# Performance work log

Measured on AMD Instinct MI355X. Metric: run time of the kernel, lower is better.

The kernel has to match this reference:

```python
import jax, jax.numpy as jnp
import numpy as np

N_NODES = 100000
N_EDGES = 3200000
F_IN = 256
HID = 64
N_CLS = 16


def setup_inputs() -> dict:
    key = jax.random.key(0)
    ks = jax.random.split(key, 12)
    x = jax.random.normal(ks[0], (N_NODES, F_IN), dtype=jnp.float32)
    edge_index = jax.random.randint(ks[1], (2, N_EDGES), 0, N_NODES, dtype=jnp.int32)
    w_mul = jax.random.normal(ks[2], (N_EDGES, 1), dtype=jnp.float32)
    s1 = 1.0 / np.sqrt(F_IN)
    s2 = 1.0 / np.sqrt(HID)
    # layer 1 params
    lin1_w = jax.random.uniform(ks[3], (HID, F_IN), minval=-s1, maxval=s1, dtype=jnp.float32)
    lin1_b = jax.random.uniform(ks[4], (HID,), minval=-s1, maxval=s1, dtype=jnp.float32)
    mlp1_w0 = jax.random.uniform(ks[5], (HID, 1), minval=-1.0, maxval=1.0, dtype=jnp.float32)
    mlp1_w1 = jax.random.uniform(ks[6], (HID, HID), minval=-s2, maxval=s2, dtype=jnp.float32)
    mlp1_b1 = jax.random.uniform(ks[7], (HID,), minval=-s2, maxval=s2, dtype=jnp.float32)
    # layer 2 params
    lin2_w = jax.random.uniform(ks[8], (N_CLS, HID), minval=-s2, maxval=s2, dtype=jnp.float32)
    lin2_b = jax.random.uniform(ks[9], (N_CLS,), minval=-s2, maxval=s2, dtype=jnp.float32)
    mlp2_w0 = jax.random.uniform(ks[10], (HID, 1), minval=-1.0, maxval=1.0, dtype=jnp.float32)
    mlp2_w1 = jax.random.uniform(ks[11], (N_CLS, HID), minval=-s2, maxval=s2, dtype=jnp.float32)
    mlp2_b1 = jnp.zeros((N_CLS,), dtype=jnp.float32)
    return dict(x=x, edge_index=edge_index, w_mul=w_mul,
                lin1_w=lin1_w, lin1_b=lin1_b, mlp1_w0=mlp1_w0, mlp1_w1=mlp1_w1, mlp1_b1=mlp1_b1,
                lin2_w=lin2_w, lin2_b=lin2_b, mlp2_w0=mlp2_w0, mlp2_w1=mlp2_w1, mlp2_b1=mlp2_b1)


def curv_layer(x, src, dst, w_mul, lin_w, lin_b, m_w0, m_w1, m_b1, n_nodes):
    # dense projection: [N, out]
    h = x @ lin_w.T + lin_b
    # per-edge weight MLP: Linear(1,HID,no bias) -> LeakyReLU(0.2) -> Linear(HID,out,bias)
    ew = jax.nn.leaky_relu(w_mul @ m_w0.T, negative_slope=0.2) @ m_w1.T + m_b1  # [E, out]
    # segment softmax keyed by source node (PyG softmax(out_weight, edge_index[0]))
    emax = jax.ops.segment_max(ew, src, num_segments=n_nodes)  # [N, out]
    e = jnp.exp(ew - emax[src])
    esum = jax.ops.segment_sum(e, src, num_segments=n_nodes)
    alpha = e / (esum[src] + 1e-16)  # [E, out]
    # message = alpha * x_j (x_j = h[src]); scatter-add at destination
    msg = alpha * h[src]
    return jax.ops.segment_sum(msg, dst, num_segments=n_nodes)  # [N, out]


def reference(x, edge_index, w_mul,
              lin1_w, lin1_b, mlp1_w0, mlp1_w1, mlp1_b1,
              lin2_w, lin2_b, mlp2_w0, mlp2_w1, mlp2_b1):
    src, dst = edge_index[0], edge_index[1]
    n = x.shape[0]
    # eval mode: dropout(p=0.8) is identity
    h = curv_layer(x, src, dst, w_mul, lin1_w, lin1_b, mlp1_w0, mlp1_w1, mlp1_b1, n)
    h = jax.nn.elu(h)
    h = curv_layer(h, src, dst, w_mul, lin2_w, lin2_b, mlp2_w0, mlp2_w1, mlp2_b1, n)
    return jax.nn.log_softmax(h, axis=1)
```

## Files before the change

### kernel.cpp

```cpp
#include <hip/hip_runtime.h>
#include <math.h>

#define FIN 256
#define HID 64
#define NCLS 16
#define BSH 8
#define BWD (1 << BSH)
#define NBKMAX 512
#define CAP 9216
#define CHUNK_S 16384
#define CHUNK_D 8192

typedef __attribute__((ext_vector_type(8))) short bf16x8;
typedef __attribute__((ext_vector_type(4))) float f32x4;

__global__ __launch_bounds__(512) void init_kernel(int* gcur_s, int* gcur_d) {
    int tid = threadIdx.x;
    gcur_s[tid] = tid * CAP;
    gcur_d[tid] = tid * CAP;
}

__global__ __launch_bounds__(512) void stage_kernel(const int* __restrict__ ei,
                                                    const float* __restrict__ w,
                                                    int* gcur_s, int* gcur_d,
                                                    unsigned int* st_s, uint2* st_d,
                                                    int E, int nchunk_s) {
    __shared__ int lh[NBKMAX];
    __shared__ int lofs[NBKMAX];
    __shared__ int lcur[NBKMAX];
    __shared__ int gbase[NBKMAX];
    __shared__ uint2 buf2[CHUNK_D];
    unsigned int* buf1 = (unsigned int*)buf2;
    int tid = threadIdx.x;
    int side = (blockIdx.x >= nchunk_s) ? 1 : 0;
    lh[tid] = 0;
    __syncthreads();
    if (!side) {
        int base = blockIdx.x * CHUNK_S;
        #pragma unroll
        for (int j = 0; j < CHUNK_S / 512; j++) {
            int e = base + tid + j * 512;
            if (e < E) atomicAdd(&lh[((unsigned)ei[e]) >> BSH], 1);
        }
    } else {
        int base = (blockIdx.x - nchunk_s) * CHUNK_D;
        #pragma unroll
        for (int j = 0; j < CHUNK_D / 512; j++) {
            int e = base + tid + j * 512;
            if (e < E) atomicAdd(&lh[((unsigned)ei[E + e]) >> BSH], 1);
        }
    }
    __syncthreads();
    int v = lh[tid];
    lofs[tid] = v;
    __syncthreads();
    for (int off = 1; off < 512; off <<= 1) {
        int add = (tid >= off) ? lofs[tid - off] : 0;
        __syncthreads();
        lofs[tid] += add;
        __syncthreads();
    }
    int ex = lofs[tid] - v;
    lofs[tid] = ex;
    lcur[tid] = ex;
    __syncthreads();
    if (!side) {
        int base = blockIdx.x * CHUNK_S;
        #pragma unroll
        for (int j = 0; j < CHUNK_S / 512; j++) {
            int e = base + tid + j * 512;
            if (e < E) {
                int s = ei[e];
                unsigned int rec = (__float_as_uint(w[e]) & 0xFFFFFF00u) | (unsigned int)(s & 0xFF);
                int p = atomicAdd(&lcur[((unsigned)s) >> BSH], 1);
                buf1[p] = rec;
            }
        }
    } else {
        int base = (blockIdx.x - nchunk_s) * CHUNK_D;
        #pragma unroll
        for (int j = 0; j < CHUNK_D / 512; j++) {
            int e = base + tid + j * 512;
            if (e < E) {
                int d = ei[E + e];
                int s = ei[e];
                unsigned int rec = (__float_as_uint(w[e]) & 0xFFFFFF00u) | (unsigned int)(d & 0xFF);
                int p = atomicAdd(&lcur[((unsigned)d) >> BSH], 1);
                buf2[p] = make_uint2((unsigned int)s, rec);
            }
        }
    }
    __syncthreads();
    {
        int c = lh[tid];
        if (c) gbase[tid] = atomicAdd(side ? &gcur_d[tid] : &gcur_s[tid], c);
    }
    __syncthreads();
    int wv = tid >> 6, lane = tid & 63;
    if (!side) {
        for (int b = wv; b < NBKMAX; b += 8) {
            int c = lh[b];
            int ls = lofs[b], gs = gbase[b];
            for (int i = lane; i < c; i += 64) st_s[gs + i] = buf1[ls + i];
        }
    } else {
        for (int b = wv; b < NBKMAX; b += 8) {
            int c = lh[b];
            int ls = lofs[b], gs = gbase[b];
            for (int i = lane; i < c; i += 64) st_d[gs + i] = buf2[ls + i];
        }
    }
}

__global__ __launch_bounds__(512) void bucket_scan_kernel(const int* gcur_s, const int* gcur_d,
                                                          int* bbase_s, int* bbase_d,
                                                          int* offs_s, int* offs_d,
                                                          int N, int nbk, int E) {
    int side = blockIdx.x;
    const int* gc = side ? gcur_d : gcur_s;
    int* bb = side ? bbase_d : bbase_s;
    __shared__ int tmp[512];
    int tid = threadIdx.x;
    int v = (tid < nbk) ? (gc[tid] - tid * CAP) : 0;
    tmp[tid] = v;
    __syncthreads();
    for (int off = 1; off < 512; off <<= 1) {
        int add = (tid >= off) ? tmp[tid - off] : 0;
        __syncthreads();
        tmp[tid] += add;
        __syncthreads();
    }
    if (tid < nbk) bb[tid] = tmp[tid] - v;
    if (tid == 0) {
        bb[nbk] = E;
        (side ? offs_d : offs_s)[N] = E;
    }
}

__global__ __launch_bounds__(256) void bucket_build_s_kernel(const int* __restrict__ bbase,
                                                             const unsigned int* __restrict__ st,
                                                             int* offs, float* t_s, int N) {
    int b = blockIdx.x;
    int r0 = bbase[b];
    int cnt = bbase[b + 1] - r0;
    if (cnt > CAP) cnt = CAP;
    size_t sb = (size_t)b * CAP;
    int n0 = b << BSH;
    int nn = min(BWD, N - n0);
    __shared__ int lh[BWD];
    __shared__ int lofs[BWD];
    __shared__ float buf[CAP];
    int tid = threadIdx.x;
    lh[tid] = 0;
    __syncthreads();
    for (int i = tid; i < cnt; i += 256) atomicAdd(&lh[st[sb + i] & 0xFFu], 1);
    __syncthreads();
    int v = lh[tid];
    lofs[tid] = v;
    __syncthreads();
    for (int off = 1; off < 256; off <<= 1) {
        int add = (tid >= off) ? lofs[tid - off] : 0;
        __syncthreads();
        lofs[tid] += add;
        __syncthreads();
    }
    int ex = lofs[tid] - v;
    if (tid < nn) offs[n0 + tid] = r0 + ex;
    lofs[tid] = ex;
    __syncthreads();
    for (int i = tid; i < cnt; i += 256) {
        unsigned int rec = st[sb + i];
        int p = atomicAdd(&lofs[rec & 0xFFu], 1);
        buf[p] = __uint_as_float(rec & 0xFFFFFF00u);
    }
    __syncthreads();
    for (int i = tid; i < cnt; i += 256) t_s[r0 + i] = buf[i];
}

__global__ __launch_bounds__(256) void bucket_build_d_kernel(const int* __restrict__ bbase,
                                                             const uint2* __restrict__ st,
                                                             int* offs, int2* ed, int N) {
    int b = blockIdx.x;
    int r0 = bbase[b];
    int cnt = bbase[b + 1] - r0;
    if (cnt > CAP) cnt = CAP;
    size_t sb = (size_t)b * CAP;
    int n0 = b << BSH;
    int nn = min(BWD, N - n0);
    __shared__ int lh[BWD];
    __shared__ int lofs[BWD];
    __shared__ int2 buf[CAP];
    int tid = threadIdx.x;
    lh[tid] = 0;
    __syncthreads();
    for (int i = tid; i < cnt; i += 256) atomicAdd(&lh[st[sb + i].y & 0xFFu], 1);
    __syncthreads();
    int v = lh[tid];
    lofs[tid] = v;
    __syncthreads();
    for (int off = 1; off < 256; off <<= 1) {
        int add = (tid >= off) ? lofs[tid - off] : 0;
        __syncthreads();
        lofs[tid] += add;
        __syncthreads();
    }
    int ex = lofs[tid] - v;
    if (tid < nn) offs[n0 + tid] = r0 + ex;
    lofs[tid] = ex;
    __syncthreads();
    for (int i = tid; i < cnt; i += 256) {
        uint2 rec = st[sb + i];
        int p = atomicAdd(&lofs[rec.y & 0xFFu], 1);
        buf[p] = make_int2((int)rec.x, (int)(rec.y & 0xFFFFFF00u));
    }
    __syncthreads();
    for (int i = tid; i < cnt; i += 256) ed[r0 + i] = buf[i];
}

#define LOG2E 1.44269504088896340736f
__global__ void prep_kernel(const float* __restrict__ w0a, const float* __restrict__ w1a,
                            const float* __restrict__ w0b, const float* __restrict__ w1b,
                            float* Ap1, float* An1, float* Ap2, float* An2) {
    int tid = threadIdx.x;
    if (tid < 64) {
        float ap = 0.f, an = 0.f;
        for (int j = 0; j < 64; j++) {
            float w0 = w0a[j];
            float w1 = w1a[tid * 64 + j];
            ap += w0 * ((w0 >= 0.f) ? 1.f : 0.2f) * w1;
            an += w0 * ((w0 <= 0.f) ? 1.f : 0.2f) * w1;
        }
        Ap1[tid] = ap * LOG2E; An1[tid] = an * LOG2E;
    } else if (tid < 80) {
        int k = tid - 64;
        float ap = 0.f, an = 0.f;
        for (int j = 0; j < 64; j++) {
            float w0 = w0b[j];
            float w1 = w1b[k * 64 + j];
            ap += w0 * ((w0 >= 0.f) ? 1.f : 0.2f) * w1;
            an += w0 * ((w0 <= 0.f) ? 1.f : 0.2f) * w1;
        }
        Ap2[k] = ap * LOG2E; An2[k] = an * LOG2E;
    }
}

__global__ __launch_bounds__(256) void esum1_kernel(const int* __restrict__ offs,
                                                    const float* __restrict__ t_s,
                                                    const float* __restrict__ Ap,
                                                    const float* __restrict__ An,
                                                    float* __restrict__ inv, int N) {
    int node = blockIdx.x * 4 + (threadIdx.x >> 6);
    int k = threadIdx.x & 63;
    if (node >= N) return;
    int s0 = offs[node], s1 = offs[node + 1];
    float ap = Ap[k], an = An[k];
    float sum = 0.f;
    int i = s0;
    for (; i + 3 < s1; i += 4) {
        float t0 = t_s[i], t1 = t_s[i + 1], t2 = t_s[i + 2], t3 = t_s[i + 3];
        sum += __builtin_amdgcn_exp2f(t0 * ((t0 >= 0.f) ? ap : an));
        sum += __builtin_amdgcn_exp2f(t1 * ((t1 >= 0.f) ? ap : an));
        sum += __builtin_amdgcn_exp2f(t2 * ((t2 >= 0.f) ? ap : an));
        sum += __builtin_amdgcn_exp2f(t3 * ((t3 >= 0.f) ? ap : an));
    }
    for (; i < s1; i++) {
        float t = t_s[i];
        sum += __builtin_amdgcn_exp2f(t * ((t >= 0.f) ? ap : an));
    }
    inv[(size_t)node * 64 + k] = (s1 > s0) ? 1.f / (sum + 1e-16f) : 0.f;
}

__global__ __launch_bounds__(256) void esum2_kernel(const int* __restrict__ offs,
                                                    const float* __restrict__ t_s,
                                                    const float* __restrict__ Ap,
                                                    const float* __restrict__ An,
                                                    float* __restrict__ inv, int N) {
    int node = blockIdx.x * 16 + (threadIdx.x >> 4);
    int k = threadIdx.x & 15;
    if (node >= N) return;
    int s0 = offs[node], s1 = offs[node + 1];
    float ap = Ap[k], an = An[k];
    float sum = 0.f;
    int i = s0;
    for (; i + 3 < s1; i += 4) {
        float t0 = t_s[i], t1 = t_s[i + 1], t2 = t_s[i + 2], t3 = t_s[i + 3];
        sum += __builtin_amdgcn_exp2f(t0 * ((t0 >= 0.f) ? ap : an));
        sum += __builtin_amdgcn_exp2f(t1 * ((t1 >= 0.f) ? ap : an));
        sum += __builtin_amdgcn_exp2f(t2 * ((t2 >= 0.f) ? ap : an));
        sum += __builtin_amdgcn_exp2f(t3 * ((t3 >= 0.f) ? ap : an));
    }
    for (; i < s1; i++) {
        float t = t_s[i];
        sum += __builtin_amdgcn_exp2f(t * ((t >= 0.f) ? ap : an));
    }
    inv[(size_t)node * 16 + k] = (s1 > s0) ? 1.f / (sum + 1e-16f) : 0.f;
}

__device__ __forceinline__ unsigned int bf16rn(float f) {
    unsigned int u = __float_as_uint(f);
    return (u + 0x7fffu + ((u >> 16) & 1u)) >> 16;
}

__device__ __forceinline__ void cvt8_split(const float4 a, const float4 b, bf16x8& h, bf16x8& l) {
    float f[8] = {a.x, a.y, a.z, a.w, b.x, b.y, b.z, b.w};
    #pragma unroll
    for (int j = 0; j < 8; j++) {
        unsigned int uh = bf16rn(f[j]);
        float hf = __uint_as_float(uh << 16);
        float r = f[j] - hf;
        unsigned int ul = bf16rn(r);
        h[j] = (short)uh;
        l[j] = (short)ul;
    }
}

#define KCH 64
__global__ __launch_bounds__(256, 4) void gemm1_kernel(const float* __restrict__ x,
                                                       const float* __restrict__ W,
                                                       const float* __restrict__ b,
                                                       const float* __restrict__ inv,
                                                       uint2* __restrict__ g1, int N) {
    __shared__ unsigned short xh[64 * KCH];
    __shared__ unsigned short xl[64 * KCH];
    __shared__ unsigned short wh[64 * KCH];
    __shared__ unsigned short wl[64 * KCH];
    int tid = threadIdx.x;
    int block_row = blockIdx.x * 64;
    float4 pf[4][2];
    auto load_chunk = [&](int kbase) {
        #pragma unroll
        for (int i = 0; i < 4; i++) {
            int t = tid + i * 256;
            if (t < 512) {
                int r = t >> 3, g = t & 7;
                int gr = block_row + r;
                if (gr < N) {
                    const float* p = &x[(size_t)gr * FIN + kbase + g * 8];
                    pf[i][0] = *(const float4*)p;
                    pf[i][1] = *(const float4*)(p + 4);
                } else {
                    pf[i][0] = make_float4(0.f, 0.f, 0.f, 0.f);
                    pf[i][1] = make_float4(0.f, 0.f, 0.f, 0.f);
                }
            } else {
                int r = (t - 512) >> 3, g = t & 7;
                const float* p = &W[r * FIN + kbase + g * 8];
                pf[i][0] = *(const float4*)p;
                pf[i][1] = *(const float4*)(p + 4);
            }
        }
    };
    auto write_chunk = [&]() {
        #pragma unroll
        for (int i = 0; i < 4; i++) {
            int t = tid + i * 256;
            int r = (t & 511) >> 3, g = t & 7;
            int gs = g ^ (r & 7);
            bf16x8 h, l;
            cvt8_split(pf[i][0], pf[i][1], h, l);
            if (t < 512) {
                *(bf16x8*)&xh[r * KCH + gs * 8] = h;
                *(bf16x8*)&xl[r * KCH + gs * 8] = l;
            } else {
                *(bf16x8*)&wh[r * KCH + gs * 8] = h;
                *(bf16x8*)&wl[r * KCH + gs * 8] = l;
            }
        }
    };

    int wv = tid >> 6, l = tid & 63;
    int lrow = l & 15, kg = l >> 4;
    f32x4 acc[4];
    #pragma unroll
    for (int c = 0; c < 4; c++) acc[c] = (f32x4){0.f, 0.f, 0.f, 0.f};

    const unsigned short* xrow_h = &xh[(wv * 16 + lrow) * KCH];
    const unsigned short* xrow_l = &xl[(wv * 16 + lrow) * KCH];

    load_chunk(0);
    for (int kc = 0; kc < FIN / KCH; kc++) {
        write_chunk();
        __syncthreads();
        if (kc + 1 < FIN / KCH) load_chunk((kc + 1) * KCH);
        #pragma unroll
        for (int s = 0; s < 2; s++) {
            int gB = ((s * 4 + kg) ^ (lrow & 7)) * 8;
            bf16x8 bh = *(const bf16x8*)&xrow_h[gB];
            bf16x8 bl = *(const bf16x8*)&xrow_l[gB];
            #pragma unroll
            for (int c = 0; c < 4; c++) {
                int wro = (c * 16 + lrow) * KCH + gB;
                bf16x8 ah = *(const bf16x8*)&wh[wro];
                bf16x8 al = *(const bf16x8*)&wl[wro];
                acc[c] = __builtin_amdgcn_mfma_f32_16x16x32_bf16(ah, bh, acc[c], 0, 0, 0);
                acc[c] = __builtin_amdgcn_mfma_f32_16x16x32_bf16(ah, bl, acc[c], 0, 0, 0);
                acc[c] = __builtin_amdgcn_mfma_f32_16x16x32_bf16(al, bh, acc[c], 0, 0, 0);
            }
        }
        __syncthreads();
    }
    int node = block_row + wv * 16 + lrow;
    if (node < N) {
        #pragma unroll
        for (int c = 0; c < 4; c++) {
            int colb = c * 16 + kg * 4;
            float4 bv = *(const float4*)&b[colb];
            float4 iv = *(const float4*)&inv[(size_t)node * 64 + colb];
            float o0 = (acc[c].x + bv.x) * iv.x;
            float o1 = (acc[c].y + bv.y) * iv.y;
            float o2 = (acc[c].z + bv.z) * iv.z;
            float o3 = (acc[c].w + bv.w) * iv.w;
            uint2 p;
            p.x = bf16rn(o0) | (bf16rn(o1) << 16);
            p.y = bf16rn(o2) | (bf16rn(o3) << 16);
            g1[(size_t)node * 16 + (colb >> 2)] = p;
        }
    }
}

#define GP 68
__global__ __launch_bounds__(256) void gemm2_kernel(const float* __restrict__ x2,
                                                    const float* __restrict__ W2,
                                                    const float* __restrict__ b2,
                                                    const float* __restrict__ inv,
                                                    float* __restrict__ g2, int N) {
    __shared__ float ws[16][GP];
    __shared__ float xs[16][GP];
    __shared__ float bs[16];
    int tid = threadIdx.x;
    {
        int c = tid >> 4, j4 = tid & 15;
        float4 v = ((const float4*)W2)[tid];
        ws[c][j4 * 4 + 0] = v.x; ws[c][j4 * 4 + 1] = v.y;
        ws[c][j4 * 4 + 2] = v.z; ws[c][j4 * 4 + 3] = v.w;
    }
    if (tid < 16) bs[tid] = b2[tid];
    int node0 = blockIdx.x * 16;
    {
        int r = tid >> 4, c4 = tid & 15;
        int gn = node0 + r;
        float4 v = (gn < N) ? *(const float4*)&x2[(size_t)gn * 64 + c4 * 4]
                            : make_float4(0.f, 0.f, 0.f, 0.f);
        xs[r][c4 * 4 + 0] = v.x; xs[r][c4 * 4 + 1] = v.y;
        xs[r][c4 * 4 + 2] = v.z; xs[r][c4 * 4 + 3] = v.w;
    }
    __syncthreads();
    int node_l = tid >> 4, col = tid & 15;
    int gn = node0 + node_l;
    if (gn >= N) return;
    float acc = bs[col];
    #pragma unroll
    for (int j4 = 0; j4 < 16; j4++) {
        float4 xv = *(const float4*)&xs[node_l][j4 * 4];
        float4 wv = *(const float4*)&ws[col][j4 * 4];
        acc += xv.x * wv.x + xv.y * wv.y + xv.z * wv.z + xv.w * wv.w;
    }
    g2[(size_t)gn * NCLS + col] = acc * inv[(size_t)gn * NCLS + col];
}

__global__ __launch_bounds__(256) void agg1_kernel(const int* __restrict__ offs,
                                                   const int2* __restrict__ ed,
                                                   const float* __restrict__ Ap,
                                                   const float* __restrict__ An,
                                                   const uint4* __restrict__ g,
                                                   float* __restrict__ x2, int N) {
    int node = blockIdx.x * 32 + (threadIdx.x >> 3);
    int l = threadIdx.x & 7;
    if (node >= N) return;
    int d0 = offs[node], d1 = offs[node + 1];
    float4 ap0 = ((const float4*)Ap)[l * 2], ap1 = ((const float4*)Ap)[l * 2 + 1];
    float4 an0 = ((const float4*)An)[l * 2], an1 = ((const float4*)An)[l * 2 + 1];
    float4 acc0 = make_float4(0.f, 0.f, 0.f, 0.f);
    float4 acc1 = make_float4(0.f, 0.f, 0.f, 0.f);
    int i = d0;
    int end4 = d0 + ((d1 - d0) & ~3);
    for (; i < end4; i += 4) {
        int2 e[4];
        #pragma unroll
        for (int j = 0; j < 4; j++) e[j] = ed[i + j];
        uint4 gv[4];
        #pragma unroll
        for (int j = 0; j < 4; j++)
            gv[j] = g[((size_t)e[j].x << 3) + l];
        #pragma unroll
        for (int j = 0; j < 4; j++) {
            float t = __int_as_float(e[j].y);
            float4 a0 = (t >= 0.f) ? ap0 : an0;
            float4 a1 = (t >= 0.f) ? ap1 : an1;
            acc0.x += __builtin_amdgcn_exp2f(t * a0.x) * __uint_as_float(gv[j].x << 16);
            acc0.y += __builtin_amdgcn_exp2f(t * a0.y) * __uint_as_float(gv[j].x & 0xffff0000u);
            acc0.z += __builtin_amdgcn_exp2f(t * a0.z) * __uint_as_float(gv[j].y << 16);
            acc0.w += __builtin_amdgcn_exp2f(t * a0.w) * __uint_as_float(gv[j].y & 0xffff0000u);
            acc1.x += __builtin_amdgcn_exp2f(t * a1.x) * __uint_as_float(gv[j].z << 16);
            acc1.y += __builtin_amdgcn_exp2f(t * a1.y) * __uint_as_float(gv[j].z & 0xffff0000u);
            acc1.z += __builtin_amdgcn_exp2f(t * a1.z) * __uint_as_float(gv[j].w << 16);
            acc1.w += __builtin_amdgcn_exp2f(t * a1.w) * __uint_as_float(gv[j].w & 0xffff0000u);
        }
    }
    for (; i < d1; i++) {
        int2 e = ed[i];
        float t = __int_as_float(e.y);
        float4 a0 = (t >= 0.f) ? ap0 : an0;
        float4 a1 = (t >= 0.f) ? ap1 : an1;
        uint4 gv = g[((size_t)e.x << 3) + l];
        acc0.x += __builtin_amdgcn_exp2f(t * a0.x) * __uint_as_float(gv.x << 16);
        acc0.y += __builtin_amdgcn_exp2f(t * a0.y) * __uint_as_float(gv.x & 0xffff0000u);
        acc0.z += __builtin_amdgcn_exp2f(t * a0.z) * __uint_as_float(gv.y << 16);
        acc0.w += __builtin_amdgcn_exp2f(t * a0.w) * __uint_as_float(gv.y & 0xffff0000u);
        acc1.x += __builtin_amdgcn_exp2f(t * a1.x) * __uint_as_float(gv.z << 16);
        acc1.y += __builtin_amdgcn_exp2f(t * a1.y) * __uint_as_float(gv.z & 0xffff0000u);
        acc1.z += __builtin_amdgcn_exp2f(t * a1.z) * __uint_as_float(gv.w << 16);
        acc1.w += __builtin_amdgcn_exp2f(t * a1.w) * __uint_as_float(gv.w & 0xffff0000u);
    }
    float4 o0, o1;
    o0.x = (acc0.x > 0.f) ? acc0.x : (__expf(acc0.x) - 1.f);
    o0.y = (acc0.y > 0.f) ? acc0.y : (__expf(acc0.y) - 1.f);
    o0.z = (acc0.z > 0.f) ? acc0.z : (__expf(acc0.z) - 1.f);
    o0.w = (acc0.w > 0.f) ? acc0.w : (__expf(acc0.w) - 1.f);
    o1.x = (acc1.x > 0.f) ? acc1.x : (__expf(acc1.x) - 1.f);
    o1.y = (acc1.y > 0.f) ? acc1.y : (__expf(acc1.y) - 1.f);
    o1.z = (acc1.z > 0.f) ? acc1.z : (__expf(acc1.z) - 1.f);
    o1.w = (acc1.w > 0.f) ? acc1.w : (__expf(acc1.w) - 1.f);
    float* dst = x2 + ((size_t)node << 6) + l * 8;
    *(float4*)(dst) = o0;
    *(float4*)(dst + 4) = o1;
}

__global__ __launch_bounds__(256) void agg2_kernel(const int* __restrict__ offs,
                                                   const int2* __restrict__ ed,
                                                   const float* __restrict__ Ap,
                                                   const float* __restrict__ An,
                                                   const float* __restrict__ g,
                                                   float* __restrict__ out, int N) {
    int node = blockIdx.x * 64 + (threadIdx.x >> 2);
    int l = threadIdx.x & 3;
    if (node >= N) return;
    int d0 = offs[node], d1 = offs[node + 1];
    float4 ap = ((const float4*)Ap)[l];
    float4 an = ((const float4*)An)[l];
    float4 acc = make_float4(0.f, 0.f, 0.f, 0.f);
    int i = d0;
    int end8 = d0 + ((d1 - d0) & ~7);
    for (; i < end8; i += 8) {
        int2 e[8];
        #pragma unroll
        for (int j = 0; j < 8; j++) e[j] = ed[i + j];
        float4 gv[8];
        #pragma unroll
        for (int j = 0; j < 8; j++)
            gv[j] = *(const float4*)(g + ((size_t)e[j].x << 4) + l * 4);
        #pragma unroll
        for (int j = 0; j < 8; j++) {
            float t = __int_as_float(e[j].y);
            float4 a = (t >= 0.f) ? ap : an;
            acc.x += __builtin_amdgcn_exp2f(t * a.x) * gv[j].x;
            acc.y += __builtin_amdgcn_exp2f(t * a.y) * gv[j].y;
            acc.z += __builtin_amdgcn_exp2f(t * a.z) * gv[j].z;
            acc.w += __builtin_amdgcn_exp2f(t * a.w) * gv[j].w;
        }
    }
    for (; i < d1; i++) {
        int2 e = ed[i];
        float t = __int_as_float(e.y);
        float4 a = (t >= 0.f) ? ap : an;
        float4 gv = *(const float4*)(g + ((size_t)e.x << 4) + l * 4);
        acc.x += __builtin_amdgcn_exp2f(t * a.x) * gv.x;
        acc.y += __builtin_amdgcn_exp2f(t * a.y) * gv.y;
        acc.z += __builtin_amdgcn_exp2f(t * a.z) * gv.z;
        acc.w += __builtin_amdgcn_exp2f(t * a.w) * gv.w;
    }
    float m = fmaxf(fmaxf(acc.x, acc.y), fmaxf(acc.z, acc.w));
    m = fmaxf(m, __shfl_xor(m, 1, 4));
    m = fmaxf(m, __shfl_xor(m, 2, 4));
    float s = __expf(acc.x - m) + __expf(acc.y - m) + __expf(acc.z - m) + __expf(acc.w - m);
    s += __shfl_xor(s, 1, 4);
    s += __shfl_xor(s, 2, 4);
    float lse = m + __logf(s);
    float4 o = make_float4(acc.x - lse, acc.y - lse, acc.z - lse, acc.w - lse);
    *(float4*)(out + ((size_t)node << 4) + l * 4) = o;
}

extern "C" void kernel_launch(void* const* d_in, const int* in_sizes, int n_in,
                              void* d_out, int out_size, void* d_ws, size_t ws_size,
                              hipStream_t stream) {
    const float* x      = (const float*)d_in[0];
    const int*   ei     = (const int*)d_in[1];
    const float* wmul   = (const float*)d_in[2];
    const float* lin1_w = (const float*)d_in[3];
    const float* lin1_b = (const float*)d_in[4];
    const float* m1w0   = (const float*)d_in[5];
    const float* m1w1   = (const float*)d_in[6];
    const float* lin2_w = (const float*)d_in[8];
    const float* lin2_b = (const float*)d_in[9];
    const float* m2w0   = (const float*)d_in[10];
    const float* m2w1   = (const float*)d_in[11];

    int N = in_sizes[0] / FIN;
    int E = in_sizes[1] / 2;
    int nbk = (N + BWD - 1) >> BSH;
    int nchunk_s = (E + CHUNK_S - 1) / CHUNK_S;
    int nchunk_d = (E + CHUNK_D - 1) / CHUNK_D;

    char* ws = (char*)d_ws;
    auto alloc = [&](size_t bytes) {
        char* p = ws;
        ws += (bytes + 255) & ~(size_t)255;
        return p;
    };
    int*   gcur_s  = (int*)alloc(NBKMAX * 4);
    int*   gcur_d  = (int*)alloc(NBKMAX * 4);
    int*   bbase_s = (int*)alloc((NBKMAX + 1) * 4);
    int*   bbase_d = (int*)alloc((NBKMAX + 1) * 4);
    float* Ap1     = (float*)alloc(64 * 4);
    float* An1     = (float*)alloc(64 * 4);
    float* Ap2     = (float*)alloc(16 * 4);
    float* An2     = (float*)alloc(16 * 4);
    int*   offs_s  = (int*)alloc((size_t)(N + 1) * 4);
    int*   offs_d  = (int*)alloc((size_t)(N + 1) * 4);
    float* t_s     = (float*)alloc((size_t)E * 4);
    int2*  ed      = (int2*)alloc((size_t)E * 8);
    char*  reg = ws;
    unsigned int* st_s = (unsigned int*)(reg);
    uint2*        st_d = (uint2*)(reg + (((size_t)nbk * CAP * 4 + 255) & ~(size_t)255));
    float* inv1 = (float*)(reg);
    float* x2   = (float*)(reg);
    char*  regB = reg + (((size_t)N * 64 * 4 + 255) & ~(size_t)255);
    uint2* g1   = (uint2*)(regB);
    float* inv2 = (float*)(regB + ((size_t)N * 16 * 8));
    float* g2   = (float*)(regB + ((size_t)N * 16 * 8) + ((size_t)N * 16 * 4));

    init_kernel<<<1, 512, 0, stream>>>(gcur_s, gcur_d);
    prep_kernel<<<1, 128, 0, stream>>>(m1w0, m1w1, m2w0, m2w1, Ap1, An1, Ap2, An2);
    stage_kernel<<<nchunk_s + nchunk_d, 512, 0, stream>>>(ei, wmul, gcur_s, gcur_d,
                                                          st_s, st_d, E, nchunk_s);
    bucket_scan_kernel<<<2, 512, 0, stream>>>(gcur_s, gcur_d, bbase_s, bbase_d,
                                              offs_s, offs_d, N, nbk, E);
    bucket_build_s_kernel<<<nbk, 256, 0, stream>>>(bbase_s, st_s, offs_s, t_s, N);
    bucket_build_d_kernel<<<nbk, 256, 0, stream>>>(bbase_d, st_d, offs_d, ed, N);
    esum1_kernel<<<(N + 3) / 4, 256, 0, stream>>>(offs_s, t_s, Ap1, An1, inv1, N);
    gemm1_kernel<<<(N + 63) / 64, 256, 0, stream>>>(x, lin1_w, lin1_b, inv1, g1, N);
    agg1_kernel<<<(N + 31) / 32, 256, 0, stream>>>(offs_d, ed, Ap1, An1, (const uint4*)g1, x2, N);
    esum2_kernel<<<(N + 15) / 16, 256, 0, stream>>>(offs_s, t_s, Ap2, An2, inv2, N);
    gemm2_kernel<<<(N + 15) / 16, 256, 0, stream>>>(x2, lin2_w, lin2_b, inv2, g2, N);
    agg2_kernel<<<(N + 63) / 64, 256, 0, stream>>>(offs_d, ed, Ap2, An2, g2, (float*)d_out, N);
}
```

Measured before the change: 500.0 us.

## Fuse both esum passes and speed up edge staging scan and copy-out

The two per-node softmax denominator kernels are merged into one that reads each source-sorted edge weight once. The first 16 lanes of each node's 64-lane group also accumulate the layer-2 sums, which removes one kernel launch and a second pass over t_s. The staging kernel's block-wide Hillis-Steele scan is replaced by a wave-shuffle scan plus a per-wave prefix. Its chunk sizes are halved for more blocks and less LDS per block. Bucket copy-out now uses 16-lane groups per bucket, so small buckets leave fewer lanes idle, at the cost of divergence in the layer-1 esum waves and more global atomics on the bucket cursors.

```diff
diff --git a/kernel.cpp b/kernel.cpp
--- a/kernel.cpp
+++ b/kernel.cpp
@@ -8,8 +8,8 @@
 #define BWD (1 << BSH)
 #define NBKMAX 512
 #define CAP 9216
-#define CHUNK_S 16384
-#define CHUNK_D 8192
+#define CHUNK_S 8192
+#define CHUNK_D 4096
 
 typedef __attribute__((ext_vector_type(8))) short bf16x8;
 typedef __attribute__((ext_vector_type(4))) float f32x4;
@@ -29,9 +29,11 @@
     __shared__ int lofs[NBKMAX];
     __shared__ int lcur[NBKMAX];
     __shared__ int gbase[NBKMAX];
+    __shared__ int wsum[8];
     __shared__ uint2 buf2[CHUNK_D];
     unsigned int* buf1 = (unsigned int*)buf2;
     int tid = threadIdx.x;
+    int wv = tid >> 6, lane = tid & 63;
     int side = (blockIdx.x >= nchunk_s) ? 1 : 0;
     lh[tid] = 0;
     __syncthreads();
@@ -52,15 +54,18 @@
     }
     __syncthreads();
     int v = lh[tid];
-    lofs[tid] = v;
-    __syncthreads();
-    for (int off = 1; off < 512; off <<= 1) {
-        int add = (tid >= off) ? lofs[tid - off] : 0;
-        __syncthreads();
-        lofs[tid] += add;
-        __syncthreads();
-    }
-    int ex = lofs[tid] - v;
+    int inc = v;
+    #pragma unroll
+    for (int off = 1; off < 64; off <<= 1) {
+        int p = __shfl_up(inc, off);
+        if (lane >= off) inc += p;
+    }
+    if (lane == 63) wsum[wv] = inc;
+    __syncthreads();
+    int pre = 0;
+    #pragma unroll
+    for (int j = 0; j < 8; j++) pre += (j < wv) ? wsum[j] : 0;
+    int ex = pre + inc - v;
     lofs[tid] = ex;
     lcur[tid] = ex;
     __syncthreads();
@@ -96,18 +101,20 @@
         if (c) gbase[tid] = atomicAdd(side ? &gcur_d[tid] : &gcur_s[tid], c);
     }
     __syncthreads();
-    int wv = tid >> 6, lane = tid & 63;
+    int sub = lane >> 4, ln = lane & 15;
     if (!side) {
-        for (int b = wv; b < NBKMAX; b += 8) {
+        for (int b0 = wv * 64; b0 < wv * 64 + 64; b0 += 4) {
+            int b = b0 + sub;
             int c = lh[b];
             int ls = lofs[b], gs = gbase[b];
-            for (int i = lane; i < c; i += 64) st_s[gs + i] = buf1[ls + i];
+            for (int i = ln; i < c; i += 16) st_s[gs + i] = buf1[ls + i];
         }
     } else {
-        for (int b = wv; b < NBKMAX; b += 8) {
+        for (int b0 = wv * 64; b0 < wv * 64 + 64; b0 += 4) {
+            int b = b0 + sub;
             int c = lh[b];
             int ls = lofs[b], gs = gbase[b];
-            for (int i = lane; i < c; i += 64) st_d[gs + i] = buf2[ls + i];
+            for (int i = ln; i < c; i += 16) st_d[gs + i] = buf2[ls + i];
         }
     }
 }
@@ -244,17 +251,23 @@
     }
 }
 
-__global__ __launch_bounds__(256) void esum1_kernel(const int* __restrict__ offs,
-                                                    const float* __restrict__ t_s,
-                                                    const float* __restrict__ Ap,
-                                                    const float* __restrict__ An,
-                                                    float* __restrict__ inv, int N) {
+__global__ __launch_bounds__(256) void esum_kernel(const int* __restrict__ offs,
+                                                   const float* __restrict__ t_s,
+                                                   const float* __restrict__ Ap1,
+                                                   const float* __restrict__ An1,
+                                                   const float* __restrict__ Ap2,
+                                                   const float* __restrict__ An2,
+                                                   float* __restrict__ inv1,
+                                                   float* __restrict__ inv2, int N) {
     int node = blockIdx.x * 4 + (threadIdx.x >> 6);
     int k = threadIdx.x & 63;
     if (node >= N) return;
     int s0 = offs[node], s1 = offs[node + 1];
-    float ap = Ap[k], an = An[k];
-    float sum = 0.f;
+    float ap = Ap1[k], an = An1[k];
+    bool lo = (k < 16);
+    float ap2 = lo ? Ap2[k] : 0.f;
+    float an2 = lo ? An2[k] : 0.f;
+    float sum = 0.f, sum2 = 0.f;
     int i = s0;
     for (; i + 3 < s1; i += 4) {
         float t0 = t_s[i], t1 = t_s[i + 1], t2 = t_s[i + 2], t3 = t_s[i + 3];
@@ -262,38 +275,20 @@
         sum += __builtin_amdgcn_exp2f(t1 * ((t1 >= 0.f) ? ap : an));
         sum += __builtin_amdgcn_exp2f(t2 * ((t2 >= 0.f) ? ap : an));
         sum += __builtin_amdgcn_exp2f(t3 * ((t3 >= 0.f) ? ap : an));
+        if (lo) {
+            sum2 += __builtin_amdgcn_exp2f(t0 * ((t0 >= 0.f) ? ap2 : an2));
+            sum2 += __builtin_amdgcn_exp2f(t1 * ((t1 >= 0.f) ? ap2 : an2));
+            sum2 += __builtin_amdgcn_exp2f(t2 * ((t2 >= 0.f) ? ap2 : an2));
+            sum2 += __builtin_amdgcn_exp2f(t3 * ((t3 >= 0.f) ? ap2 : an2));
+        }
     }
     for (; i < s1; i++) {
         float t = t_s[i];
         sum += __builtin_amdgcn_exp2f(t * ((t >= 0.f) ? ap : an));
-    }
-    inv[(size_t)node * 64 + k] = (s1 > s0) ? 1.f / (sum + 1e-16f) : 0.f;
-}
-
-__global__ __launch_bounds__(256) void esum2_kernel(const int* __restrict__ offs,
-                                                    const float* __restrict__ t_s,
-                                                    const float* __restrict__ Ap,
-                                                    const float* __restrict__ An,
-                                                    float* __restrict__ inv, int N) {
-    int node = blockIdx.x * 16 + (threadIdx.x >> 4);
-    int k = threadIdx.x & 15;
-    if (node >= N) return;
-    int s0 = offs[node], s1 = offs[node + 1];
-    float ap = Ap[k], an = An[k];
-    float sum = 0.f;
-    int i = s0;
-    for (; i + 3 < s1; i += 4) {
-        float t0 = t_s[i], t1 = t_s[i + 1], t2 = t_s[i + 2], t3 = t_s[i + 3];
-        sum += __builtin_amdgcn_exp2f(t0 * ((t0 >= 0.f) ? ap : an));
-        sum += __builtin_amdgcn_exp2f(t1 * ((t1 >= 0.f) ? ap : an));
-        sum += __builtin_amdgcn_exp2f(t2 * ((t2 >= 0.f) ? ap : an));
-        sum += __builtin_amdgcn_exp2f(t3 * ((t3 >= 0.f) ? ap : an));
-    }
-    for (; i < s1; i++) {
-        float t = t_s[i];
-        sum += __builtin_amdgcn_exp2f(t * ((t >= 0.f) ? ap : an));
-    }
-    inv[(size_t)node * 16 + k] = (s1 > s0) ? 1.f / (sum + 1e-16f) : 0.f;
+        if (lo) sum2 += __builtin_amdgcn_exp2f(t * ((t >= 0.f) ? ap2 : an2));
+    }
+    inv1[(size_t)node * 64 + k] = (s1 > s0) ? 1.f / (sum + 1e-16f) : 0.f;
+    if (lo) inv2[(size_t)node * 16 + k] = (s1 > s0) ? 1.f / (sum2 + 1e-16f) : 0.f;
 }
 
 __device__ __forceinline__ unsigned int bf16rn(float f) {
@@ -637,10 +632,9 @@
                                               offs_s, offs_d, N, nbk, E);
     bucket_build_s_kernel<<<nbk, 256, 0, stream>>>(bbase_s, st_s, offs_s, t_s, N);
     bucket_build_d_kernel<<<nbk, 256, 0, stream>>>(bbase_d, st_d, offs_d, ed, N);
-    esum1_kernel<<<(N + 3) / 4, 256, 0, stream>>>(offs_s, t_s, Ap1, An1, inv1, N);
+    esum_kernel<<<(N + 3) / 4, 256, 0, stream>>>(offs_s, t_s, Ap1, An1, Ap2, An2, inv1, inv2, N);
     gemm1_kernel<<<(N + 63) / 64, 256, 0, stream>>>(x, lin1_w, lin1_b, inv1, g1, N);
     agg1_kernel<<<(N + 31) / 32, 256, 0, stream>>>(offs_d, ed, Ap1, An1, (const uint4*)g1, x2, N);
-    esum2_kernel<<<(N + 15) / 16, 256, 0, stream>>>(offs_s, t_s, Ap2, An2, inv2, N);
     gemm2_kernel<<<(N + 15) / 16, 256, 0, stream>>>(x2, lin2_w, lin2_b, inv2, g2, N);
     agg2_kernel<<<(N + 63) / 64, 256, 0, stream>>>(offs_d, ed, Ap2, An2, g2, (float*)d_out, N);
 }
```

Result: faster. 485.1 us (-3.0%).
